# Optimization experiments

Hardware: AMD Instinct MI355X
Metric: run time of the kernel (lower is better)

## Reference

```python
import jax, jax.numpy as jnp
import numpy as np

N = 8192      # nodes
E = 16384     # query edges
D = 256       # node feature dim
NNZ = 262144  # overlap matrix nnz (avg degree 32)
P1, P2, P3 = 32, 32, 32


def _mlp(x, W1, b1, W2, b2):
    # Linear(1->p) -> ReLU -> Linear(p->1)
    return jax.nn.relu(x @ W1 + b1) @ W2 + b2


def setup_inputs() -> dict:
    key = jax.random.key(0)
    ks = jax.random.split(key, 16)
    inp = {
        "edges": jax.random.randint(ks[0], (E, 2), 0, N, dtype=jnp.int32),
        "row": jax.random.randint(ks[1], (NNZ,), 0, N, dtype=jnp.int32),
        "col": jax.random.randint(ks[2], (NNZ,), 0, N, dtype=jnp.int32),
        "values": jax.random.uniform(ks[3], (NNZ,), dtype=jnp.float32),
        "H": jax.random.normal(ks[4], (N, D), dtype=jnp.float32),
        # f_edge: 1 -> P1 -> 1
        "we1": jax.random.normal(ks[5], (1, P1), dtype=jnp.float32) * 0.5,
        "be1": jnp.zeros((P1,), jnp.float32),
        "we2": jax.random.normal(ks[6], (P1, 1), dtype=jnp.float32) * 0.5,
        "be2": jnp.zeros((1,), jnp.float32),
        # f_node: 1 -> P2 -> 1
        "wn1": jax.random.normal(ks[7], (1, P2), dtype=jnp.float32) * 0.5,
        "bn1": jnp.zeros((P2,), jnp.float32),
        "wn2": jax.random.normal(ks[8], (P2, 1), dtype=jnp.float32) * 0.5,
        "bn2": jnp.zeros((1,), jnp.float32),
        # psi_3: 1 -> P3 -> 1
        "wp1": jax.random.normal(ks[9], (1, P3), dtype=jnp.float32) * 0.5,
        "bp1": jnp.zeros((P3,), jnp.float32),
        "wp2": jax.random.normal(ks[10], (P3, 1), dtype=jnp.float32) * 0.5,
        "bp2": jnp.zeros((1,), jnp.float32),
        "alpha": jnp.zeros((2,), jnp.float32),
    }
    return inp


def reference(edges, row, col, values, H,
              we1, be1, we2, be2,
              wn1, bn1, wn2, bn2,
              wp1, bp1, wp2, bp2, alpha):
    src, dst = edges[:, 0], edges[:, 1]

    # --- BatchDotPred: sigmoid(<H[src], H[dst]>) ---
    h_link = jax.nn.sigmoid(jnp.einsum('ed,ed->e', H[src], H[dst]))[:, None]  # [E,1]

    # --- MultiHopAggregator ---
    edge_feat = _mlp(values[:, None], we1, be1, we2, be2)           # [NNZ,1]
    node_in = jax.ops.segment_sum(edge_feat, col, num_segments=N)  # [N,1] scatter_add over col
    struct = _mlp(node_in, wn1, bn1, wn2, bn2)[:, 0]                # [N]

    # dense overlap adjacency (coo.todense(), duplicates summed)
    adj = jnp.zeros((N, N), values.dtype).at[row, col].add(values)  # [N,N]

    # NOTE: faithful to source bug: both src and dst neighborhoods gather src rows
    sn = adj[src]                                                   # [E,N]
    agg = jnp.einsum('en,n->e', sn * sn, struct * struct)[:, None]  # [E,1]

    z_link = jax.nn.sigmoid(_mlp(agg, wp1, bp1, wp2, bp2))          # [E,1]

    a = jax.nn.softmax(alpha)
    y_hat = a[0] * z_link + a[1] * h_link + 1e-15
    return y_hat
```

## Files before the change

### kernel.cpp

```cpp
#include <hip/hip_runtime.h>
#include <math.h>

#define N_NODES 8192
#define D_DIM   256
#define E_EDGES 16384
#define NNZ_CNT 262144

#define NBLK 64
#define BTHR 1024
#define PER_BLK (NNZ_CNT / NBLK)

__device__ __forceinline__ float sigmoidf(float x) {
    return 1.0f / (1.0f + expf(-x));
}

__global__ void k_stage(const int* __restrict__ col,
                        const float* __restrict__ values,
                        const float* __restrict__ we1,
                        const float* __restrict__ be1,
                        const float* __restrict__ we2,
                        const float* __restrict__ be2,
                        float* __restrict__ partial) {
    __shared__ float bins[N_NODES];
    for (int j = threadIdx.x; j < N_NODES; j += BTHR) bins[j] = 0.0f;
    __syncthreads();
    int base = blockIdx.x * PER_BLK;
#pragma unroll
    for (int it = 0; it < PER_BLK / BTHR; ++it) {
        int k = base + it * BTHR + threadIdx.x;
        float v = values[k];
        int c = col[k];
        float f = be2[0];
#pragma unroll
        for (int j = 0; j < 32; ++j) {
            float t = fmaf(v, we1[j], be1[j]);
            t = t > 0.0f ? t : 0.0f;
            f = fmaf(t, we2[j], f);
        }
        atomicAdd(&bins[c], f);
    }
    __syncthreads();
    float* p = partial + (size_t)blockIdx.x * N_NODES;
    for (int j = threadIdx.x; j < N_NODES; j += BTHR) p[j] = bins[j];
}

__global__ void k_node(const float* __restrict__ partial,
                       const float* __restrict__ wn1,
                       const float* __restrict__ bn1,
                       const float* __restrict__ wn2,
                       const float* __restrict__ bn2,
                       float* __restrict__ struct2) {
    int i = blockIdx.x * blockDim.x + threadIdx.x;
    float x = 0.0f;
#pragma unroll 8
    for (int b = 0; b < NBLK; ++b) x += partial[(size_t)b * N_NODES + i];
    float u = bn2[0];
#pragma unroll
    for (int j = 0; j < 32; ++j) {
        float t = fmaf(x, wn1[j], bn1[j]);
        t = t > 0.0f ? t : 0.0f;
        u = fmaf(t, wn2[j], u);
    }
    struct2[i] = u * u;
}

__global__ void k_raccum(const int* __restrict__ row,
                         const int* __restrict__ col,
                         const float* __restrict__ values,
                         const float* __restrict__ struct2,
                         float* __restrict__ partial) {
    __shared__ float bins[N_NODES];
    for (int j = threadIdx.x; j < N_NODES; j += BTHR) bins[j] = 0.0f;
    __syncthreads();
    int base = blockIdx.x * PER_BLK;
#pragma unroll
    for (int it = 0; it < PER_BLK / BTHR; ++it) {
        int k = base + it * BTHR + threadIdx.x;
        float v = values[k];
        int r = row[k];
        int c = col[k];
        atomicAdd(&bins[r], v * v * struct2[c]);
    }
    __syncthreads();
    float* p = partial + (size_t)blockIdx.x * N_NODES;
    for (int j = threadIdx.x; j < N_NODES; j += BTHR) p[j] = bins[j];
}

__global__ void k_rreduce(const float* __restrict__ partial,
                          float* __restrict__ r) {
    int i = blockIdx.x * blockDim.x + threadIdx.x;
    float x = 0.0f;
#pragma unroll 8
    for (int b = 0; b < NBLK; ++b) x += partial[(size_t)b * N_NODES + i];
    r[i] = x;
}

__global__ void k_final(const int* __restrict__ edges,
                        const float* __restrict__ H,
                        const float* __restrict__ r,
                        const float* __restrict__ wp1,
                        const float* __restrict__ bp1,
                        const float* __restrict__ wp2,
                        const float* __restrict__ bp2,
                        const float* __restrict__ alpha,
                        float* __restrict__ out) {
    int e = blockIdx.x * (blockDim.x >> 6) + (threadIdx.x >> 6);
    int lane = threadIdx.x & 63;
    if (e >= E_EDGES) return;
    int src = edges[2 * e];
    int dst = edges[2 * e + 1];
    const float4* H4 = (const float4*)H;
    float4 a4 = H4[src * (D_DIM / 4) + lane];
    float4 b4 = H4[dst * (D_DIM / 4) + lane];
    float dot = a4.x * b4.x + a4.y * b4.y + a4.z * b4.z + a4.w * b4.w;
#pragma unroll
    for (int off = 32; off >= 1; off >>= 1)
        dot += __shfl_xor(dot, off, 64);
    if (lane == 0) {
        float h = sigmoidf(dot);
        float agg = r[src];
        float u = bp2[0];
#pragma unroll
        for (int j = 0; j < 32; ++j) {
            float t = fmaf(agg, wp1[j], bp1[j]);
            t = t > 0.0f ? t : 0.0f;
            u = fmaf(t, wp2[j], u);
        }
        float z = sigmoidf(u);
        float m = fmaxf(alpha[0], alpha[1]);
        float e0 = expf(alpha[0] - m);
        float e1 = expf(alpha[1] - m);
        float inv = 1.0f / (e0 + e1);
        out[e] = (e0 * inv) * z + (e1 * inv) * h + 1e-15f;
    }
}

extern "C" void kernel_launch(void* const* d_in, const int* in_sizes, int n_in,
                              void* d_out, int out_size, void* d_ws, size_t ws_size,
                              hipStream_t stream) {
    const int*   edges  = (const int*)d_in[0];
    const int*   row    = (const int*)d_in[1];
    const int*   col    = (const int*)d_in[2];
    const float* values = (const float*)d_in[3];
    const float* H      = (const float*)d_in[4];
    const float* we1    = (const float*)d_in[5];
    const float* be1    = (const float*)d_in[6];
    const float* we2    = (const float*)d_in[7];
    const float* be2    = (const float*)d_in[8];
    const float* wn1    = (const float*)d_in[9];
    const float* bn1    = (const float*)d_in[10];
    const float* wn2    = (const float*)d_in[11];
    const float* bn2    = (const float*)d_in[12];
    const float* wp1    = (const float*)d_in[13];
    const float* bp1    = (const float*)d_in[14];
    const float* wp2    = (const float*)d_in[15];
    const float* bp2    = (const float*)d_in[16];
    const float* alpha  = (const float*)d_in[17];
    float* out = (float*)d_out;

    float* ws_f    = (float*)d_ws;
    float* partial = ws_f;
    float* struct2 = ws_f + (size_t)NBLK * N_NODES;
    float* rbuf    = struct2 + N_NODES;

    k_stage<<<NBLK, BTHR, 0, stream>>>(col, values, we1, be1, we2, be2, partial);
    k_node<<<N_NODES / 1024, 1024, 0, stream>>>(partial, wn1, bn1, wn2, bn2, struct2);
    k_raccum<<<NBLK, BTHR, 0, stream>>>(row, col, values, struct2, partial);
    k_rreduce<<<N_NODES / 1024, 1024, 0, stream>>>(partial, rbuf);
    k_final<<<E_EDGES / 4, 256, 0, stream>>>(edges, H, rbuf, wp1, bp1, wp2, bp2, alpha, out);
}
```

Baseline: 132.5 us.

## Fuse all stages into one cooperative kernel with grid syncs

Replaces the five separate kernel launches with a single cooperative kernel of 256 blocks that separates the phases with grid.sync. It also raises the block count from 64 to 256 so the per-block histogram and reduction phases spread across more CUs. The edge dot products are computed in the first phase alongside the histogram, overlapping that work with it. In exchange it adds grid-wide barriers, writes a 4x larger partial buffer (256 x 8192 floats) that must be reduced, and needs all 256 blocks of 1024 threads with 32KB of LDS each to be co-resident.

Measured after the change: 260.5 us. +96.6%, slower.

```diff
diff --git a/kernel.cpp b/kernel.cpp
--- a/kernel.cpp
+++ b/kernel.cpp
@@ -1,33 +1,48 @@
 #include <hip/hip_runtime.h>
+#include <hip/hip_cooperative_groups.h>
 #include <math.h>
+
+namespace cg = cooperative_groups;
 
 #define N_NODES 8192
 #define D_DIM   256
 #define E_EDGES 16384
 #define NNZ_CNT 262144
 
-#define NBLK 64
-#define BTHR 1024
-#define PER_BLK (NNZ_CNT / NBLK)
+#define NB 256
+#define BT 1024
+#define NNZ_PB (NNZ_CNT / NB)
+#define EDG_PB (E_EDGES / NB)
+#define NODE_PB (N_NODES / NB)
 
 __device__ __forceinline__ float sigmoidf(float x) {
     return 1.0f / (1.0f + expf(-x));
 }
 
-__global__ void k_stage(const int* __restrict__ col,
-                        const float* __restrict__ values,
-                        const float* __restrict__ we1,
-                        const float* __restrict__ be1,
-                        const float* __restrict__ we2,
-                        const float* __restrict__ be2,
-                        float* __restrict__ partial) {
+__global__ __launch_bounds__(BT, 4) void k_fused(
+    const int* __restrict__ edges, const int* __restrict__ row,
+    const int* __restrict__ col, const float* __restrict__ values,
+    const float* __restrict__ H,
+    const float* __restrict__ we1, const float* __restrict__ be1,
+    const float* __restrict__ we2, const float* __restrict__ be2,
+    const float* __restrict__ wn1, const float* __restrict__ bn1,
+    const float* __restrict__ wn2, const float* __restrict__ bn2,
+    const float* __restrict__ wp1, const float* __restrict__ bp1,
+    const float* __restrict__ wp2, const float* __restrict__ bp2,
+    const float* __restrict__ alpha,
+    float* __restrict__ partial, float* __restrict__ struct2,
+    float* __restrict__ rbuf, float* __restrict__ hbuf,
+    float* __restrict__ out)
+{
+    cg::grid_group grid = cg::this_grid();
     __shared__ float bins[N_NODES];
-    for (int j = threadIdx.x; j < N_NODES; j += BTHR) bins[j] = 0.0f;
-    __syncthreads();
-    int base = blockIdx.x * PER_BLK;
-#pragma unroll
-    for (int it = 0; it < PER_BLK / BTHR; ++it) {
-        int k = base + it * BTHR + threadIdx.x;
+    const int tid = threadIdx.x;
+    const int bid = blockIdx.x;
+
+    for (int j = tid; j < N_NODES; j += BT) bins[j] = 0.0f;
+    __syncthreads();
+    {
+        int k = bid * NNZ_PB + tid;
         float v = values[k];
         int c = col[k];
         float f = be2[0];
@@ -39,86 +54,95 @@
         }
         atomicAdd(&bins[c], f);
     }
-    __syncthreads();
-    float* p = partial + (size_t)blockIdx.x * N_NODES;
-    for (int j = threadIdx.x; j < N_NODES; j += BTHR) p[j] = bins[j];
-}
-
-__global__ void k_node(const float* __restrict__ partial,
-                       const float* __restrict__ wn1,
-                       const float* __restrict__ bn1,
-                       const float* __restrict__ wn2,
-                       const float* __restrict__ bn2,
-                       float* __restrict__ struct2) {
-    int i = blockIdx.x * blockDim.x + threadIdx.x;
-    float x = 0.0f;
-#pragma unroll 8
-    for (int b = 0; b < NBLK; ++b) x += partial[(size_t)b * N_NODES + i];
-    float u = bn2[0];
-#pragma unroll
-    for (int j = 0; j < 32; ++j) {
-        float t = fmaf(x, wn1[j], bn1[j]);
-        t = t > 0.0f ? t : 0.0f;
-        u = fmaf(t, wn2[j], u);
-    }
-    struct2[i] = u * u;
-}
-
-__global__ void k_raccum(const int* __restrict__ row,
-                         const int* __restrict__ col,
-                         const float* __restrict__ values,
-                         const float* __restrict__ struct2,
-                         float* __restrict__ partial) {
-    __shared__ float bins[N_NODES];
-    for (int j = threadIdx.x; j < N_NODES; j += BTHR) bins[j] = 0.0f;
-    __syncthreads();
-    int base = blockIdx.x * PER_BLK;
-#pragma unroll
-    for (int it = 0; it < PER_BLK / BTHR; ++it) {
-        int k = base + it * BTHR + threadIdx.x;
+    {
+        int wave = tid >> 6, lane = tid & 63;
+        const float4* H4 = (const float4*)H;
+#pragma unroll
+        for (int i = 0; i < 4; ++i) {
+            int e = bid * EDG_PB + wave * 4 + i;
+            int src = edges[2 * e];
+            int dst = edges[2 * e + 1];
+            float4 a4 = H4[src * (D_DIM / 4) + lane];
+            float4 b4 = H4[dst * (D_DIM / 4) + lane];
+            float dot = a4.x * b4.x + a4.y * b4.y + a4.z * b4.z + a4.w * b4.w;
+#pragma unroll
+            for (int off = 32; off >= 1; off >>= 1)
+                dot += __shfl_xor(dot, off, 64);
+            if (lane == 0) hbuf[e] = sigmoidf(dot);
+        }
+    }
+    __syncthreads();
+    {
+        float* p = partial + (size_t)bid * N_NODES;
+        for (int j = tid; j < N_NODES; j += BT) p[j] = bins[j];
+    }
+    grid.sync();
+
+    {
+        int sub = tid & 31;
+        int g = tid >> 5;
+        int i = bid * NODE_PB + sub;
+        float x = 0.0f;
+#pragma unroll
+        for (int j = 0; j < 8; ++j)
+            x += partial[(size_t)(g * 8 + j) * N_NODES + i];
+        bins[tid] = x;
+    }
+    __syncthreads();
+    if (tid < NODE_PB) {
+        int i = bid * NODE_PB + tid;
+        float x = 0.0f;
+#pragma unroll
+        for (int b = 0; b < 32; ++b) x += bins[b * 32 + tid];
+        float u = bn2[0];
+#pragma unroll
+        for (int j = 0; j < 32; ++j) {
+            float t = fmaf(x, wn1[j], bn1[j]);
+            t = t > 0.0f ? t : 0.0f;
+            u = fmaf(t, wn2[j], u);
+        }
+        struct2[i] = u * u;
+    }
+    grid.sync();
+
+    for (int j = tid; j < N_NODES; j += BT) bins[j] = 0.0f;
+    __syncthreads();
+    {
+        int k = bid * NNZ_PB + tid;
         float v = values[k];
-        int r = row[k];
-        int c = col[k];
-        atomicAdd(&bins[r], v * v * struct2[c]);
-    }
-    __syncthreads();
-    float* p = partial + (size_t)blockIdx.x * N_NODES;
-    for (int j = threadIdx.x; j < N_NODES; j += BTHR) p[j] = bins[j];
-}
-
-__global__ void k_rreduce(const float* __restrict__ partial,
-                          float* __restrict__ r) {
-    int i = blockIdx.x * blockDim.x + threadIdx.x;
-    float x = 0.0f;
-#pragma unroll 8
-    for (int b = 0; b < NBLK; ++b) x += partial[(size_t)b * N_NODES + i];
-    r[i] = x;
-}
-
-__global__ void k_final(const int* __restrict__ edges,
-                        const float* __restrict__ H,
-                        const float* __restrict__ r,
-                        const float* __restrict__ wp1,
-                        const float* __restrict__ bp1,
-                        const float* __restrict__ wp2,
-                        const float* __restrict__ bp2,
-                        const float* __restrict__ alpha,
-                        float* __restrict__ out) {
-    int e = blockIdx.x * (blockDim.x >> 6) + (threadIdx.x >> 6);
-    int lane = threadIdx.x & 63;
-    if (e >= E_EDGES) return;
-    int src = edges[2 * e];
-    int dst = edges[2 * e + 1];
-    const float4* H4 = (const float4*)H;
-    float4 a4 = H4[src * (D_DIM / 4) + lane];
-    float4 b4 = H4[dst * (D_DIM / 4) + lane];
-    float dot = a4.x * b4.x + a4.y * b4.y + a4.z * b4.z + a4.w * b4.w;
-#pragma unroll
-    for (int off = 32; off >= 1; off >>= 1)
-        dot += __shfl_xor(dot, off, 64);
-    if (lane == 0) {
-        float h = sigmoidf(dot);
-        float agg = r[src];
+        atomicAdd(&bins[row[k]], v * v * struct2[col[k]]);
+    }
+    __syncthreads();
+    {
+        float* p = partial + (size_t)bid * N_NODES;
+        for (int j = tid; j < N_NODES; j += BT) p[j] = bins[j];
+    }
+    grid.sync();
+
+    {
+        int sub = tid & 31;
+        int g = tid >> 5;
+        int i = bid * NODE_PB + sub;
+        float x = 0.0f;
+#pragma unroll
+        for (int j = 0; j < 8; ++j)
+            x += partial[(size_t)(g * 8 + j) * N_NODES + i];
+        bins[tid] = x;
+    }
+    __syncthreads();
+    if (tid < NODE_PB) {
+        int i = bid * NODE_PB + tid;
+        float x = 0.0f;
+#pragma unroll
+        for (int b = 0; b < 32; ++b) x += bins[b * 32 + tid];
+        rbuf[i] = x;
+    }
+    grid.sync();
+
+    if (tid < EDG_PB) {
+        int e = bid * EDG_PB + tid;
+        int src = edges[2 * e];
+        float agg = rbuf[src];
         float u = bp2[0];
 #pragma unroll
         for (int j = 0; j < 32; ++j) {
@@ -127,9 +151,11 @@
             u = fmaf(t, wp2[j], u);
         }
         float z = sigmoidf(u);
-        float m = fmaxf(alpha[0], alpha[1]);
-        float e0 = expf(alpha[0] - m);
-        float e1 = expf(alpha[1] - m);
+        float h = hbuf[e];
+        float a0 = alpha[0], a1 = alpha[1];
+        float m = fmaxf(a0, a1);
+        float e0 = expf(a0 - m);
+        float e1 = expf(a1 - m);
         float inv = 1.0f / (e0 + e1);
         out[e] = (e0 * inv) * z + (e1 * inv) * h + 1e-15f;
     }
@@ -156,16 +182,21 @@
     const float* wp2    = (const float*)d_in[15];
     const float* bp2    = (const float*)d_in[16];
     const float* alpha  = (const float*)d_in[17];
-    float* out = (float*)d_out;
+    float* outf = (float*)d_out;
 
     float* ws_f    = (float*)d_ws;
     float* partial = ws_f;
-    float* struct2 = ws_f + (size_t)NBLK * N_NODES;
+    float* struct2 = ws_f + (size_t)NB * N_NODES;
     float* rbuf    = struct2 + N_NODES;
-
-    k_stage<<<NBLK, BTHR, 0, stream>>>(col, values, we1, be1, we2, be2, partial);
-    k_node<<<N_NODES / 1024, 1024, 0, stream>>>(partial, wn1, bn1, wn2, bn2, struct2);
-    k_raccum<<<NBLK, BTHR, 0, stream>>>(row, col, values, struct2, partial);
-    k_rreduce<<<N_NODES / 1024, 1024, 0, stream>>>(partial, rbuf);
-    k_final<<<E_EDGES / 4, 256, 0, stream>>>(edges, H, rbuf, wp1, bp1, wp2, bp2, alpha, out);
+    float* hbuf    = rbuf + N_NODES;
+
+    void* args[] = { (void*)&edges, (void*)&row, (void*)&col, (void*)&values,
+                     (void*)&H,
+                     (void*)&we1, (void*)&be1, (void*)&we2, (void*)&be2,
+                     (void*)&wn1, (void*)&bn1, (void*)&wn2, (void*)&bn2,
+                     (void*)&wp1, (void*)&bp1, (void*)&wp2, (void*)&bp2,
+                     (void*)&alpha,
+                     (void*)&partial, (void*)&struct2, (void*)&rbuf,
+                     (void*)&hbuf, (void*)&outf };
+    hipLaunchCooperativeKernel((void*)k_fused, dim3(NB), dim3(BT), args, 0, stream);
 }
```
